# Optimization experiments

Hardware: AMD Instinct MI355X
Metric: run time of the kernel (lower is better)

## Reference

```python
import jax, jax.numpy as jnp
import numpy as np

N_NODES = 100000
N_EDGES = 1600000
EMB = 128
N_LAYERS = 3
BN_EPS = 1e-5


def setup_inputs() -> dict:
    key = jax.random.key(0)
    k1, k2, k3 = jax.random.split(key, 3)
    feats = jax.random.normal(k1, (N_NODES, EMB), dtype=jnp.float32)
    edge_index = jax.random.randint(k2, (2, N_EDGES), 0, N_NODES, dtype=jnp.int64)
    # Glorot-ish scaled weights per layer
    W = jax.random.normal(k3, (N_LAYERS, EMB, EMB), dtype=jnp.float32) * (1.0 / np.sqrt(EMB))
    b = jnp.zeros((N_LAYERS, EMB), dtype=jnp.float32)
    gamma = jnp.ones((N_LAYERS, EMB), dtype=jnp.float32)
    beta = jnp.zeros((N_LAYERS, EMB), dtype=jnp.float32)
    return {"feats": feats, "edge_index": edge_index, "W": W, "b": b, "gamma": gamma, "beta": beta}


def _gcn_layer(h, row, col, W_l, b_l):
    # GCNConv (add_self_loops=False, normalize=True): x = h @ W, symmetric-norm scatter-add, + bias
    x = h @ W_l  # [N, D]
    ones = jnp.ones((row.shape[0],), dtype=h.dtype)
    deg = jax.ops.segment_sum(ones, col, num_segments=N_NODES)  # in-degree of targets
    dinv = jnp.where(deg > 0, jax.lax.rsqrt(jnp.maximum(deg, 1.0)), 0.0)
    norm = dinv[row] * dinv[col]  # [E]
    msg = x[row] * norm[:, None]  # gather + scale, [E, D]
    out = jax.ops.segment_sum(msg, col, num_segments=N_NODES)  # scatter-add
    return out + b_l


def _batch_norm(h, gamma_l, beta_l):
    mu = jnp.mean(h, axis=0)
    var = jnp.mean(jnp.square(h - mu), axis=0)  # biased var (torch BN training math)
    return (h - mu) * jax.lax.rsqrt(var + BN_EPS) * gamma_l + beta_l


def reference(feats, edge_index, W, b, gamma, beta):
    row, col = edge_index[0], edge_index[1]  # source, target
    h = feats
    for l in range(N_LAYERS):
        h = _gcn_layer(h, row, col, W[l], b[l])
        h = _batch_norm(h, gamma[l], beta[l])
        # dropout treated as identity (eval mode); residual=False; JK='last'
    return h
```

## Files before the change

kernel.cpp:

```cpp
#include <hip/hip_runtime.h>
#include <cstdint>
#include <cstddef>

#define BN_EPS 1e-5f
#define NCHUNK 256

typedef short bf16x8 __attribute__((ext_vector_type(8)));
typedef float f32x4 __attribute__((ext_vector_type(4)));


__device__ __forceinline__ int edge_at(const void* e, long long i, int m64) {
  return m64 ? (int)((const long long*)e)[i] : ((const int*)e)[i];
}

__device__ __forceinline__ unsigned short f2bf(float f) {
  unsigned int u = __float_as_uint(f);
  unsigned int r = (u + 0x7FFFu + ((u >> 16) & 1u)) >> 16;
  return (unsigned short)r;
}

__device__ __forceinline__ unsigned int pack2bf(float lo, float hi) {
  return (unsigned int)f2bf(lo) | ((unsigned int)f2bf(hi) << 16);
}

__global__ void detect_kernel(const int* __restrict__ e, int* __restrict__ mode) {
  int nz = 0;
  for (int i = 1; i < 512; i += 2) nz |= e[i];
  mode[0] = (nz == 0) ? 1 : 0;
}


__global__ __launch_bounds__(256) void count_kernel(const void* __restrict__ edges,
                                                    const int* __restrict__ mode,
                                                    int* __restrict__ blockcounts,
                                                    int E, int nb, int chunk) {
  __shared__ int h[1024];
  int m = mode[0];
  for (int i = threadIdx.x; i < nb; i += 256) h[i] = 0;
  __syncthreads();
  long long lo = (long long)blockIdx.x * chunk;
  long long hi = lo + chunk;
  if (hi > E) hi = E;
  for (long long i = lo + threadIdx.x; i < hi; i += 256) {
    int c = edge_at(edges, (long long)E + i, m);
    atomicAdd(&h[c >> 8], 1);
  }
  __syncthreads();
  for (int j = threadIdx.x; j < nb; j += 256)
    blockcounts[(size_t)j * NCHUNK + blockIdx.x] = h[j];
}

__global__ __launch_bounds__(256) void scan1_kernel(const int* __restrict__ src,
                                                    int* __restrict__ tprefix,
                                                    int* __restrict__ bsum, int n) {
  __shared__ int s[256];
  int t = threadIdx.x;
  int gid = blockIdx.x * 256 + t;
  int base = gid * 4;
  int sum = 0;
#pragma unroll
  for (int j = 0; j < 4; j++) {
    int i = base + j;
    if (i < n) sum += src[i];
  }
  s[t] = sum;
  __syncthreads();
  for (int off = 1; off < 256; off <<= 1) {
    int v = (t >= off) ? s[t - off] : 0;
    __syncthreads();
    s[t] += v;
    __syncthreads();
  }
  tprefix[gid] = s[t] - sum;
  if (t == 255) bsum[blockIdx.x] = s[255];
}

__global__ __launch_bounds__(256) void scan2_kernel(int* __restrict__ bsum, int nbk,
                                                    int* __restrict__ out, int n) {
  __shared__ int s[256];
  int t = threadIdx.x;
  int v = (t < nbk) ? bsum[t] : 0;
  s[t] = v;
  __syncthreads();
  for (int off = 1; off < 256; off <<= 1) {
    int u = (t >= off) ? s[t - off] : 0;
    __syncthreads();
    s[t] += u;
    __syncthreads();
  }
  if (t < nbk) bsum[t] = s[t] - v;
  if (t == 255) out[n] = s[255];
}

__global__ __launch_bounds__(256) void scan3_kernel(const int* __restrict__ src,
                                                    const int* __restrict__ tprefix,
                                                    const int* __restrict__ bsum,
                                                    int* __restrict__ out, int n) {
  int gid = blockIdx.x * 256 + threadIdx.x;
  int run = bsum[blockIdx.x] + tprefix[gid];
  int base = gid * 4;
#pragma unroll
  for (int j = 0; j < 4; j++) {
    int i = base + j;
    if (i < n) {
      int c = src[i];
      out[i] = run;
      run += c;
    }
  }
}

__global__ __launch_bounds__(256) void scatter_kernel(const void* __restrict__ edges,
                                                      const int* __restrict__ mode,
                                                      const int* __restrict__ moff,
                                                      int* __restrict__ pairs,
                                                      int E, int nb, int chunk) {
  __shared__ int cur[1024];
  int m = mode[0];
  for (int j = threadIdx.x; j < nb; j += 256)
    cur[j] = moff[(size_t)j * NCHUNK + blockIdx.x];
  __syncthreads();
  long long lo = (long long)blockIdx.x * chunk;
  long long hi = lo + chunk;
  if (hi > E) hi = E;
  for (long long i = lo + threadIdx.x; i < hi; i += 256) {
    int r = edge_at(edges, i, m);
    int c = edge_at(edges, (long long)E + i, m);
    int pos = atomicAdd(&cur[c >> 8], 1);
    pairs[pos] = (r << 8) | (c & 255);
  }
}

__global__ __launch_bounds__(256) void passB12_kernel(const int* __restrict__ pairs,
                                                      const int* __restrict__ moff,
                                                      float* __restrict__ dinv,
                                                      int* __restrict__ offsets,
                                                      int* __restrict__ csr_row, int n) {
  __shared__ int h[256];
  __shared__ int s[256];
  int t = threadIdx.x;
  int b = blockIdx.x;
  h[t] = 0;
  __syncthreads();
  int lo = moff[(size_t)b * NCHUNK];
  int hi = moff[(size_t)(b + 1) * NCHUNK];
  for (int e = lo + t; e < hi; e += 256)
    atomicAdd(&h[pairs[e] & 255], 1);
  __syncthreads();
  int d = h[t];
  s[t] = d;
  __syncthreads();
  for (int off = 1; off < 256; off <<= 1) {
    int v = (t >= off) ? s[t - off] : 0;
    __syncthreads();
    s[t] += v;
    __syncthreads();
  }
  int start = lo + s[t] - d;
  int node = b * 256 + t;
  if (node < n) {
    offsets[node] = start;
    dinv[node] = d > 0 ? rsqrtf((float)d) : 0.f;
    if (node == n - 1) offsets[n] = hi;
  }
  s[t] = start;
  __syncthreads();
  for (int e = lo + t; e < hi; e += 256) {
    int p = pairs[e];
    int pos = atomicAdd(&s[p & 255], 1);
    csr_row[pos] = p >> 8;
  }
}

__global__ __launch_bounds__(256) void prepWR_kernel(const float* __restrict__ W,
                                                     const float* __restrict__ colstats,
                                                     const float* __restrict__ gamma,
                                                     const float* __restrict__ beta,
                                                     float invN, int use_affine,
                                                     unsigned short* __restrict__ Wt,
                                                     float* __restrict__ rbias) {
  __shared__ float sc[128], sh[128];
  int t = threadIdx.x;
  if (t < 128) {
    float scv = 1.f, shv = 0.f;
    if (use_affine) {
      float mu = colstats[t] * invN;
      float var = colstats[128 + t] * invN - mu * mu;
      var = fmaxf(var, 0.f);
      scv = gamma[t] * rsqrtf(var + BN_EPS);
      shv = beta[t] - mu * scv;
    }
    sc[t] = scv;
    sh[t] = shv;
  }
  __syncthreads();
  int idx = blockIdx.x * 256 + t;
  int nc = idx >> 7, k = idx & 127;
  Wt[(size_t)nc * 128 + k] = f2bf(W[(size_t)k * 128 + nc] * sc[k]);
  if (blockIdx.x == 0 && t < 128) {
    float s = 0.f;
    if (use_affine) {
      for (int kk = 0; kk < 128; kk++) s += sh[kk] * W[(size_t)kk * 128 + t];
    }
    rbias[t] = s;
  }
}

template <int A_IS_FP32>
__global__ __launch_bounds__(256) void gemm_mfma_kernel(
    const void* __restrict__ Ain, const unsigned short* __restrict__ Wt,
    const float* __restrict__ rbias, const float* __restrict__ dinv,
    unsigned short* __restrict__ xb, int n) {
  int l = threadIdx.x & 63;
  int w = threadIdx.x >> 6;
  int row0 = blockIdx.x * 64 + w * 16;
  int am = row0 + (l & 15);
  int amc = am < n ? am : n - 1;
  int kg = l >> 4;

  f32x4 acc[8];
#pragma unroll
  for (int nt = 0; nt < 8; nt++) {
    f32x4 zv = {0.f, 0.f, 0.f, 0.f};
    acc[nt] = zv;
  }

#pragma unroll
  for (int kk = 0; kk < 4; kk++) {
    bf16x8 a;
    if (A_IS_FP32) {
      const float* ap = (const float*)Ain + (size_t)amc * 128 + kk * 32 + kg * 8;
      float4 f0 = *(const float4*)ap;
      float4 f1 = *(const float4*)(ap + 4);
      a[0] = (short)f2bf(f0.x); a[1] = (short)f2bf(f0.y);
      a[2] = (short)f2bf(f0.z); a[3] = (short)f2bf(f0.w);
      a[4] = (short)f2bf(f1.x); a[5] = (short)f2bf(f1.y);
      a[6] = (short)f2bf(f1.z); a[7] = (short)f2bf(f1.w);
    } else {
      a = *(const bf16x8*)((const unsigned short*)Ain + (size_t)amc * 128 + kk * 32 + kg * 8);
    }
#pragma unroll
    for (int nt = 0; nt < 8; nt++) {
      bf16x8 b = *(const bf16x8*)(Wt + (size_t)(nt * 16 + (l & 15)) * 128 + kk * 32 + kg * 8);
      acc[nt] = __builtin_amdgcn_mfma_f32_16x16x32_bf16(a, b, acc[nt], 0, 0, 0);
    }
  }

  int col0 = l & 15;
  int rbase = row0 + (l >> 4) * 4;
  float dv[4];
#pragma unroll
  for (int r = 0; r < 4; r++) {
    int rr = rbase + r;
    dv[r] = dinv[rr < n ? rr : n - 1];
  }
#pragma unroll
  for (int nt = 0; nt < 8; nt++) {
    float rb = rbias[nt * 16 + col0];
#pragma unroll
    for (int r = 0; r < 4; r++) {
      int rr = rbase + r;
      if (rr < n)
        xb[(size_t)rr * 128 + nt * 16 + col0] = f2bf((acc[nt][r] + rb) * dv[r]);
    }
  }
}

template <int F32OUT>
__global__ __launch_bounds__(256, 4) void agg_kernel(
    const uint4* __restrict__ x4, const int* __restrict__ csr_row,
    const int* __restrict__ offsets, const float* __restrict__ dinv,
    void* __restrict__ z, int n) {
  int node = blockIdx.x * 16 + (threadIdx.x >> 4);
  int d8 = threadIdx.x & 15;
  if (node >= n) return;
  int lo = offsets[node], hi = offsets[node + 1];
  float a0[8] = {}, a1[8] = {}, a2[8] = {}, a3[8] = {};
#define ACC8(A, v)                                                         \
  A[0] += __uint_as_float((v).x << 16); A[1] += __uint_as_float((v).x & 0xffff0000u); \
  A[2] += __uint_as_float((v).y << 16); A[3] += __uint_as_float((v).y & 0xffff0000u); \
  A[4] += __uint_as_float((v).z << 16); A[5] += __uint_as_float((v).z & 0xffff0000u); \
  A[6] += __uint_as_float((v).w << 16); A[7] += __uint_as_float((v).w & 0xffff0000u);
  int e = lo;
  for (; e + 8 <= hi; e += 8) {
    int r0 = csr_row[e];
    int r1 = csr_row[e + 1];
    int r2 = csr_row[e + 2];
    int r3 = csr_row[e + 3];
    int r4 = csr_row[e + 4];
    int r5 = csr_row[e + 5];
    int r6 = csr_row[e + 6];
    int r7 = csr_row[e + 7];
    uint4 v0 = x4[(size_t)r0 * 16 + d8];
    uint4 v1 = x4[(size_t)r1 * 16 + d8];
    uint4 v2 = x4[(size_t)r2 * 16 + d8];
    uint4 v3 = x4[(size_t)r3 * 16 + d8];
    uint4 v4 = x4[(size_t)r4 * 16 + d8];
    uint4 v5 = x4[(size_t)r5 * 16 + d8];
    uint4 v6 = x4[(size_t)r6 * 16 + d8];
    uint4 v7 = x4[(size_t)r7 * 16 + d8];
    ACC8(a0, v0) ACC8(a1, v1) ACC8(a2, v2) ACC8(a3, v3)
    ACC8(a0, v4) ACC8(a1, v5) ACC8(a2, v6) ACC8(a3, v7)
  }
  for (; e + 4 <= hi; e += 4) {
    int r0 = csr_row[e];
    int r1 = csr_row[e + 1];
    int r2 = csr_row[e + 2];
    int r3 = csr_row[e + 3];
    uint4 v0 = x4[(size_t)r0 * 16 + d8];
    uint4 v1 = x4[(size_t)r1 * 16 + d8];
    uint4 v2 = x4[(size_t)r2 * 16 + d8];
    uint4 v3 = x4[(size_t)r3 * 16 + d8];
    ACC8(a0, v0) ACC8(a1, v1) ACC8(a2, v2) ACC8(a3, v3)
  }
  for (; e < hi; e++) {
    uint4 v = x4[(size_t)csr_row[e] * 16 + d8];
    ACC8(a0, v)
  }
#undef ACC8
  float dvn = dinv[node];
  float s[8];
#pragma unroll
  for (int j = 0; j < 8; j++) s[j] = (a0[j] + a1[j] + a2[j] + a3[j]) * dvn;
  if (F32OUT) {
    float* zp = (float*)z + (size_t)node * 128 + d8 * 8;
    *(float4*)zp = make_float4(s[0], s[1], s[2], s[3]);
    *(float4*)(zp + 4) = make_float4(s[4], s[5], s[6], s[7]);
  } else {
    uint4 o = make_uint4(pack2bf(s[0], s[1]), pack2bf(s[2], s[3]),
                         pack2bf(s[4], s[5]), pack2bf(s[6], s[7]));
    *(uint4*)((unsigned short*)z + (size_t)node * 128 + d8 * 8) = o;
  }
}

template <int F32IN>
__global__ __launch_bounds__(256) void stats2_kernel(
    const void* __restrict__ z, float* __restrict__ partial, int total8) {
  __shared__ float ps[256];
  int t = threadIdx.x;
  ps[t] = 0.f;
  __syncthreads();
  int d8 = t & 15;
  float s[8] = {}, q[8] = {};
  int idx = blockIdx.x * 256 + t;
  int stride = gridDim.x * 256;
  for (int i = idx; i < total8; i += stride) {
    float v[8];
    if (F32IN) {
      const float* zp = (const float*)z + (size_t)i * 8;
      float4 f0 = *(const float4*)zp;
      float4 f1 = *(const float4*)(zp + 4);
      v[0] = f0.x; v[1] = f0.y; v[2] = f0.z; v[3] = f0.w;
      v[4] = f1.x; v[5] = f1.y; v[6] = f1.z; v[7] = f1.w;
    } else {
      uint4 u = ((const uint4*)z)[i];
      v[0] = __uint_as_float(u.x << 16); v[1] = __uint_as_float(u.x & 0xffff0000u);
      v[2] = __uint_as_float(u.y << 16); v[3] = __uint_as_float(u.y & 0xffff0000u);
      v[4] = __uint_as_float(u.z << 16); v[5] = __uint_as_float(u.z & 0xffff0000u);
      v[6] = __uint_as_float(u.w << 16); v[7] = __uint_as_float(u.w & 0xffff0000u);
    }
#pragma unroll
    for (int j = 0; j < 8; j++) { s[j] += v[j]; q[j] += v[j] * v[j]; }
  }
#pragma unroll
  for (int j = 0; j < 8; j++) {
    atomicAdd(&ps[d8 * 8 + j], s[j]);
    atomicAdd(&ps[128 + d8 * 8 + j], q[j]);
  }
  __syncthreads();
  partial[(size_t)blockIdx.x * 256 + t] = ps[t];
}

__global__ __launch_bounds__(256) void reduce_stats_kernel(
    const float* __restrict__ partial, float* __restrict__ out, int nblk) {
  __shared__ float red[256];
  int c = blockIdx.x;
  float s = 0.f;
  for (int i = threadIdx.x; i < nblk; i += 256) s += partial[(size_t)i * 256 + c];
  red[threadIdx.x] = s;
  __syncthreads();
  for (int o = 128; o > 0; o >>= 1) {
    if (threadIdx.x < o) red[threadIdx.x] += red[threadIdx.x + o];
    __syncthreads();
  }
  if (threadIdx.x == 0) out[c] = red[0];
}

__global__ __launch_bounds__(256) void norm_kernel(
    float* __restrict__ z, const float* __restrict__ colstats,
    const float* __restrict__ gamma, const float* __restrict__ beta,
    float invN, int total4) {
  __shared__ float sc[128], sh[128];
  int t = threadIdx.x;
  if (t < 128) {
    float mu = colstats[t] * invN;
    float var = colstats[128 + t] * invN - mu * mu;
    var = fmaxf(var, 0.f);
    float s = gamma[t] * rsqrtf(var + BN_EPS);
    sc[t] = s;
    sh[t] = beta[t] - mu * s;
  }
  __syncthreads();
  int idx = blockIdx.x * blockDim.x + t;
  int stride = gridDim.x * blockDim.x;
  for (int i = idx; i < total4; i += stride) {
    float4 v = ((const float4*)z)[i];
    int d0 = (i & 31) * 4;
    v.x = v.x * sc[d0] + sh[d0];
    v.y = v.y * sc[d0 + 1] + sh[d0 + 1];
    v.z = v.z * sc[d0 + 2] + sh[d0 + 2];
    v.w = v.w * sc[d0 + 3] + sh[d0 + 3];
    ((float4*)z)[i] = v;
  }
}


extern "C" void kernel_launch(void* const* d_in, const int* in_sizes, int n_in,
                              void* d_out, int out_size, void* d_ws, size_t ws_size,
                              hipStream_t stream) {
  const float* feats = (const float*)d_in[0];
  const void* edges = d_in[1];
  const float* W = (const float*)d_in[2];
  const float* gamma = (const float*)d_in[4];
  const float* beta = (const float*)d_in[5];

  const int n = in_sizes[0] / 128;
  const int E = in_sizes[1] / 2;

  const int nb = (n + 255) / 256;
  const int m = nb * NCHUNK;
  const int chunk = (E + NCHUNK - 1) / NCHUNK;
  const int sb_m = (m + 1023) / 1024;
  const int nagg = (n + 15) / 16;
  const int nstat = 1024;

  char* ws = (char*)d_ws;
  size_t off = 0;
  unsigned short* xb = (unsigned short*)(ws + off); off += (size_t)n * 128 * 2; off = (off + 255) & ~(size_t)255;
  float* dinv = (float*)(ws + off); off += (size_t)n * 4;
  int* offsets = (int*)(ws + off); off += (size_t)(n + 1) * 4; off = (off + 255) & ~(size_t)255;
  int* csr_row = (int*)(ws + off); off += (size_t)E * 4; off = (off + 255) & ~(size_t)255;
  int* pairs = (int*)(ws + off); off += (size_t)E * 4; off = (off + 255) & ~(size_t)255;
  int* blockcounts = (int*)(ws + off); off += (size_t)m * 4; off = (off + 255) & ~(size_t)255;
  int* moff = (int*)(ws + off); off += (size_t)(m + 1) * 4; off = (off + 255) & ~(size_t)255;
  int* tprefix = (int*)(ws + off); off += (size_t)sb_m * 256 * 4; off = (off + 255) & ~(size_t)255;
  int* bsum = (int*)(ws + off); off += 256 * 4;
  unsigned short* Wt = (unsigned short*)(ws + off); off += 128 * 128 * 2; off = (off + 255) & ~(size_t)255;
  float* rbias = (float*)(ws + off); off += 128 * 4;
  float* colstats = (float*)(ws + off); off += 256 * 4;
  int* mode = (int*)(ws + off); off += 4;

  float* partial = (float*)pairs;

  detect_kernel<<<1, 1, 0, stream>>>((const int*)edges, mode);
  count_kernel<<<NCHUNK, 256, 0, stream>>>(edges, mode, blockcounts, E, nb, chunk);
  scan1_kernel<<<sb_m, 256, 0, stream>>>(blockcounts, tprefix, bsum, m);
  scan2_kernel<<<1, 256, 0, stream>>>(bsum, sb_m, moff, m);
  scan3_kernel<<<sb_m, 256, 0, stream>>>(blockcounts, tprefix, bsum, moff, m);
  scatter_kernel<<<NCHUNK, 256, 0, stream>>>(edges, mode, moff, pairs, E, nb, chunk);
  passB12_kernel<<<nb, 256, 0, stream>>>(pairs, moff, dinv, offsets, csr_row, n);

  unsigned short* zb = (unsigned short*)d_out;
  float* zf = (float*)d_out;
  const int ggrid = (n + 63) / 64;
  const int total8 = n * 16;
  const float invN = 1.0f / (float)n;

  for (int l = 0; l < 3; l++) {
    prepWR_kernel<<<64, 256, 0, stream>>>(W + (size_t)l * 16384, colstats,
                                          gamma + l * 128, beta + l * 128, invN,
                                          l > 0 ? 1 : 0, Wt, rbias);
    if (l == 0)
      gemm_mfma_kernel<1><<<ggrid, 256, 0, stream>>>(feats, Wt, rbias, dinv, xb, n);
    else
      gemm_mfma_kernel<0><<<ggrid, 256, 0, stream>>>(zb, Wt, rbias, dinv, xb, n);
    if (l < 2) {
      agg_kernel<0><<<nagg, 256, 0, stream>>>(
          (const uint4*)xb, csr_row, offsets, dinv, zb, n);
      stats2_kernel<0><<<nstat, 256, 0, stream>>>(zb, partial, total8);
    } else {
      agg_kernel<1><<<nagg, 256, 0, stream>>>(
          (const uint4*)xb, csr_row, offsets, dinv, zf, n);
      stats2_kernel<1><<<nstat, 256, 0, stream>>>(zf, partial, total8);
    }
    reduce_stats_kernel<<<256, 256, 0, stream>>>(partial, colstats, nstat);
  }
  norm_kernel<<<2048, 256, 0, stream>>>(zf, colstats, gamma + 2 * 128, beta + 2 * 128,
                                        invN, (n * 128) / 4);
}
```

Before: 485.1 us.

## Split node features into two column halves and aggregate each half separately

The GEMM now writes its bf16 output as two separate 64-column arrays, and aggregation runs as two passes, one per half, each using 8 threads per node. The aim is to shrink the gathered working set per pass to 12.8 MB so random neighbour gathers hit in L2/MALL cache more often. The cost is reading the CSR indices twice, an extra kernel launch per layer, and the removal of the 8-wide unroll and the occupancy hint in the aggregation kernel.

Measured after the change: 500.9 us. 3.3% more time.

```diff
diff --git a/kernel.cpp b/kernel.cpp
--- a/kernel.cpp
+++ b/kernel.cpp
@@ -210,7 +210,7 @@
 __global__ __launch_bounds__(256) void gemm_mfma_kernel(
     const void* __restrict__ Ain, const unsigned short* __restrict__ Wt,
     const float* __restrict__ rbias, const float* __restrict__ dinv,
-    unsigned short* __restrict__ xb, int n) {
+    unsigned short* __restrict__ xh0, unsigned short* __restrict__ xh1, int n) {
   int l = threadIdx.x & 63;
   int w = threadIdx.x >> 6;
   int row0 = blockIdx.x * 64 + w * 16;
@@ -257,22 +257,24 @@
 #pragma unroll
   for (int nt = 0; nt < 8; nt++) {
     float rb = rbias[nt * 16 + col0];
+    unsigned short* xh = (nt < 4) ? xh0 : xh1;
+    int cc = (nt & 3) * 16 + col0;
 #pragma unroll
     for (int r = 0; r < 4; r++) {
       int rr = rbase + r;
       if (rr < n)
-        xb[(size_t)rr * 128 + nt * 16 + col0] = f2bf((acc[nt][r] + rb) * dv[r]);
+        xh[(size_t)rr * 64 + cc] = f2bf((acc[nt][r] + rb) * dv[r]);
     }
   }
 }
 
 template <int F32OUT>
-__global__ __launch_bounds__(256, 4) void agg_kernel(
-    const uint4* __restrict__ x4, const int* __restrict__ csr_row,
+__global__ __launch_bounds__(256) void agg_kernel(
+    const uint4* __restrict__ xh, const int* __restrict__ csr_row,
     const int* __restrict__ offsets, const float* __restrict__ dinv,
-    void* __restrict__ z, int n) {
-  int node = blockIdx.x * 16 + (threadIdx.x >> 4);
-  int d8 = threadIdx.x & 15;
+    void* __restrict__ z, int half, int n) {
+  int node = blockIdx.x * 32 + (threadIdx.x >> 3);
+  int j = threadIdx.x & 7;
   if (node >= n) return;
   int lo = offsets[node], hi = offsets[node + 1];
   float a0[8] = {}, a1[8] = {}, a2[8] = {}, a3[8] = {};
@@ -282,54 +284,34 @@
   A[4] += __uint_as_float((v).z << 16); A[5] += __uint_as_float((v).z & 0xffff0000u); \
   A[6] += __uint_as_float((v).w << 16); A[7] += __uint_as_float((v).w & 0xffff0000u);
   int e = lo;
-  for (; e + 8 <= hi; e += 8) {
-    int r0 = csr_row[e];
-    int r1 = csr_row[e + 1];
-    int r2 = csr_row[e + 2];
-    int r3 = csr_row[e + 3];
-    int r4 = csr_row[e + 4];
-    int r5 = csr_row[e + 5];
-    int r6 = csr_row[e + 6];
-    int r7 = csr_row[e + 7];
-    uint4 v0 = x4[(size_t)r0 * 16 + d8];
-    uint4 v1 = x4[(size_t)r1 * 16 + d8];
-    uint4 v2 = x4[(size_t)r2 * 16 + d8];
-    uint4 v3 = x4[(size_t)r3 * 16 + d8];
-    uint4 v4 = x4[(size_t)r4 * 16 + d8];
-    uint4 v5 = x4[(size_t)r5 * 16 + d8];
-    uint4 v6 = x4[(size_t)r6 * 16 + d8];
-    uint4 v7 = x4[(size_t)r7 * 16 + d8];
-    ACC8(a0, v0) ACC8(a1, v1) ACC8(a2, v2) ACC8(a3, v3)
-    ACC8(a0, v4) ACC8(a1, v5) ACC8(a2, v6) ACC8(a3, v7)
-  }
   for (; e + 4 <= hi; e += 4) {
     int r0 = csr_row[e];
     int r1 = csr_row[e + 1];
     int r2 = csr_row[e + 2];
     int r3 = csr_row[e + 3];
-    uint4 v0 = x4[(size_t)r0 * 16 + d8];
-    uint4 v1 = x4[(size_t)r1 * 16 + d8];
-    uint4 v2 = x4[(size_t)r2 * 16 + d8];
-    uint4 v3 = x4[(size_t)r3 * 16 + d8];
+    uint4 v0 = xh[(size_t)r0 * 8 + j];
+    uint4 v1 = xh[(size_t)r1 * 8 + j];
+    uint4 v2 = xh[(size_t)r2 * 8 + j];
+    uint4 v3 = xh[(size_t)r3 * 8 + j];
     ACC8(a0, v0) ACC8(a1, v1) ACC8(a2, v2) ACC8(a3, v3)
   }
   for (; e < hi; e++) {
-    uint4 v = x4[(size_t)csr_row[e] * 16 + d8];
+    uint4 v = xh[(size_t)csr_row[e] * 8 + j];
     ACC8(a0, v)
   }
 #undef ACC8
   float dvn = dinv[node];
   float s[8];
 #pragma unroll
-  for (int j = 0; j < 8; j++) s[j] = (a0[j] + a1[j] + a2[j] + a3[j]) * dvn;
+  for (int jj = 0; jj < 8; jj++) s[jj] = (a0[jj] + a1[jj] + a2[jj] + a3[jj]) * dvn;
   if (F32OUT) {
-    float* zp = (float*)z + (size_t)node * 128 + d8 * 8;
+    float* zp = (float*)z + (size_t)node * 128 + half * 64 + j * 8;
     *(float4*)zp = make_float4(s[0], s[1], s[2], s[3]);
     *(float4*)(zp + 4) = make_float4(s[4], s[5], s[6], s[7]);
   } else {
     uint4 o = make_uint4(pack2bf(s[0], s[1]), pack2bf(s[2], s[3]),
                          pack2bf(s[4], s[5]), pack2bf(s[6], s[7]));
-    *(uint4*)((unsigned short*)z + (size_t)node * 128 + d8 * 8) = o;
+    *(uint4*)((unsigned short*)z + (size_t)node * 128 + half * 64 + j * 8) = o;
   }
 }
 
@@ -360,12 +342,12 @@
       v[6] = __uint_as_float(u.w << 16); v[7] = __uint_as_float(u.w & 0xffff0000u);
     }
 #pragma unroll
-    for (int j = 0; j < 8; j++) { s[j] += v[j]; q[j] += v[j] * v[j]; }
-  }
-#pragma unroll
-  for (int j = 0; j < 8; j++) {
-    atomicAdd(&ps[d8 * 8 + j], s[j]);
-    atomicAdd(&ps[128 + d8 * 8 + j], q[j]);
+    for (int jj = 0; jj < 8; jj++) { s[jj] += v[jj]; q[jj] += v[jj] * v[jj]; }
+  }
+#pragma unroll
+  for (int jj = 0; jj < 8; jj++) {
+    atomicAdd(&ps[d8 * 8 + jj], s[jj]);
+    atomicAdd(&ps[128 + d8 * 8 + jj], q[jj]);
   }
   __syncthreads();
   partial[(size_t)blockIdx.x * 256 + t] = ps[t];
@@ -431,12 +413,13 @@
   const int m = nb * NCHUNK;
   const int chunk = (E + NCHUNK - 1) / NCHUNK;
   const int sb_m = (m + 1023) / 1024;
-  const int nagg = (n + 15) / 16;
+  const int nagg = (n + 31) / 32;
   const int nstat = 1024;
 
   char* ws = (char*)d_ws;
   size_t off = 0;
-  unsigned short* xb = (unsigned short*)(ws + off); off += (size_t)n * 128 * 2; off = (off + 255) & ~(size_t)255;
+  unsigned short* xh0 = (unsigned short*)(ws + off); off += (size_t)n * 64 * 2; off = (off + 255) & ~(size_t)255;
+  unsigned short* xh1 = (unsigned short*)(ws + off); off += (size_t)n * 64 * 2; off = (off + 255) & ~(size_t)255;
   float* dinv = (float*)(ws + off); off += (size_t)n * 4;
   int* offsets = (int*)(ws + off); off += (size_t)(n + 1) * 4; off = (off + 255) & ~(size_t)255;
   int* csr_row = (int*)(ws + off); off += (size_t)E * 4; off = (off + 255) & ~(size_t)255;
@@ -471,16 +454,20 @@
                                           gamma + l * 128, beta + l * 128, invN,
                                           l > 0 ? 1 : 0, Wt, rbias);
     if (l == 0)
-      gemm_mfma_kernel<1><<<ggrid, 256, 0, stream>>>(feats, Wt, rbias, dinv, xb, n);
+      gemm_mfma_kernel<1><<<ggrid, 256, 0, stream>>>(feats, Wt, rbias, dinv, xh0, xh1, n);
     else
-      gemm_mfma_kernel<0><<<ggrid, 256, 0, stream>>>(zb, Wt, rbias, dinv, xb, n);
+      gemm_mfma_kernel<0><<<ggrid, 256, 0, stream>>>(zb, Wt, rbias, dinv, xh0, xh1, n);
     if (l < 2) {
       agg_kernel<0><<<nagg, 256, 0, stream>>>(
-          (const uint4*)xb, csr_row, offsets, dinv, zb, n);
+          (const uint4*)xh0, csr_row, offsets, dinv, zb, 0, n);
+      agg_kernel<0><<<nagg, 256, 0, stream>>>(
+          (const uint4*)xh1, csr_row, offsets, dinv, zb, 1, n);
       stats2_kernel<0><<<nstat, 256, 0, stream>>>(zb, partial, total8);
     } else {
       agg_kernel<1><<<nagg, 256, 0, stream>>>(
-          (const uint4*)xb, csr_row, offsets, dinv, zf, n);
+          (const uint4*)xh0, csr_row, offsets, dinv, zf, 0, n);
+      agg_kernel<1><<<nagg, 256, 0, stream>>>(
+          (const uint4*)xh1, csr_row, offsets, dinv, zf, 1, n);
       stats2_kernel<1><<<nstat, 256, 0, stream>>>(zf, partial, total8);
     }
     reduce_stats_kernel<<<256, 256, 0, stream>>>(partial, colstats, nstat);
```
